# Kernel optimization log

Hardware: AMD Instinct MI355X
Metric: run time of the kernel (lower is better)

Reference implementation:

```python
import jax, jax.numpy as jnp
import numpy as np
import math

B, S, L, D, H, NL, FF, MAXP = 4, 200, 256, 256, 8, 2, 1024, 512
VOC, EDIM, BERT_D, LBL = 50000, 50, 768, 20
DH = D // H
NEG = -1e15


def _pe_table():
    # get_embedding(max_seq_len, hidden, rel_pos_init=0): sinusoidal over 0..2*MAXP
    half = D // 2
    freq = jnp.exp(jnp.arange(half, dtype=jnp.float32) * (-math.log(10000.0) / (half - 1)))
    pos = jnp.arange(2 * MAXP + 1, dtype=jnp.float32)[:, None] * freq[None, :]
    return jnp.concatenate([jnp.sin(pos), jnp.cos(pos)], axis=1)  # [2*MAXP+1, D]


def _ln(x, g, b, eps=1e-5):
    m = x.mean(-1, keepdims=True)
    v = jnp.mean((x - m) ** 2, -1, keepdims=True)
    return (x - m) * jax.lax.rsqrt(v + eps) * g + b


def _forward(lattice, bigrams, seq_len, lex_num, pos_s, pos_e,
             bert_embed, lat_table, big_table, Wc, bc, Wl, bl, W_fus, b_fus,
             Wq, bq, Wk, bk, Wv, bv, Wr, br, u, vb, Wo, bo,
             ln1_g, ln1_b, W1, b1, W2, b2, ln2_g, ln2_b, Wout, bout):
    raw = lat_table[lattice]                                        # [B,L,EDIM]
    big = jnp.pad(big_table[bigrams], ((0, 0), (0, L - S), (0, 0)))  # pad to lattice len
    bert = jnp.pad(bert_embed, ((0, 0), (0, L - S), (0, 0)))
    raw_char = jnp.concatenate([raw, big, bert], -1)                # [B,L,868]
    idx = jnp.arange(L)
    char_mask = idx[None, :] < seq_len[:, None]
    tot_mask = idx[None, :] < (seq_len + lex_num)[:, None]
    lex_mask = tot_mask & (~char_mask)
    # embed_char masked to char positions, embed_lex masked to lexicon positions
    x = (raw_char @ Wc + bc) * char_mask[..., None] + (raw @ Wl + bl) * lex_mask[..., None]

    # four-way relative position fusion ('ff'): relu(Linear(cat[pe_ss,pe_se,pe_es,pe_ee]))
    # computed as sum of four gathered pre-projected tables (same math, no 4D concat)
    pe = _pe_table()
    T = jnp.einsum('pe,keo->kpo', pe, W_fus.reshape(4, D, D))       # [4, 2*MAXP+1, D]
    ss = pos_s[:, :, None] - pos_s[:, None, :] + MAXP
    se = pos_s[:, :, None] - pos_e[:, None, :] + MAXP
    es = pos_e[:, :, None] - pos_s[:, None, :] + MAXP
    ee = pos_e[:, :, None] - pos_e[:, None, :] + MAXP
    rel = jax.nn.relu(T[0][ss] + T[1][se] + T[2][es] + T[3][ee] + b_fus)  # [B,L,L,D]

    scale = 1.0 / math.sqrt(DH)
    for l in range(NL):
        qh = (x @ Wq[l] + bq[l]).reshape(B, L, H, DH).transpose(0, 2, 1, 3)
        kh = (x @ Wk[l] + bk[l]).reshape(B, L, H, DH).transpose(0, 2, 1, 3)
        vh = (x @ Wv[l] + bv[l]).reshape(B, L, H, DH).transpose(0, 2, 1, 3)
        rh = (rel @ Wr[l] + br[l]).reshape(B, L, L, H, DH)
        # Transformer-XL style: A+C with content bias u, B+D with position bias v
        AC = jnp.einsum('bhqd,bhkd->bhqk', qh + u[l][None, :, None, :], kh)
        BD = jnp.einsum('bhqd,bqkhd->bhqk', qh + vb[l][None, :, None, :], rh)
        score = (AC + BD) * scale
        score = jnp.where(tot_mask[:, None, None, :], score, NEG)
        attn = jax.nn.softmax(score, -1)
        out = jnp.einsum('bhqk,bhkd->bhqd', attn, vh).transpose(0, 2, 1, 3).reshape(B, L, D)
        x = _ln(out @ Wo[l] + bo[l] + x, ln1_g[l], ln1_b[l])
        h = jax.nn.relu(x @ W1[l] + b1[l]) @ W2[l] + b2[l]
        x = _ln(h + x, ln2_g[l], ln2_b[l])
    return x[:, :S] @ Wout + bout                                   # emission logits [B,S,LBL]


def setup_inputs() -> dict:
    key = jax.random.key(0)
    ks = jax.random.split(key, 32)
    p = lambda i, sh, s=0.02: jax.random.normal(ks[i], sh, jnp.float32) * s
    inp = {}
    inp['lattice'] = jax.random.randint(ks[0], (B, L), 1, VOC)
    inp['bigrams'] = jax.random.randint(ks[1], (B, S), 1, VOC)
    inp['seq_len'] = jax.random.randint(ks[2], (B,), 150, S + 1)
    inp['lex_num'] = jax.random.randint(ks[3], (B,), 20, L - S + 1)
    s_lex = jax.random.randint(ks[4], (B, L - S), 0, 180)
    e_lex = s_lex + jax.random.randint(ks[5], (B, L - S), 1, 20)
    ar = jnp.broadcast_to(jnp.arange(S), (B, S))
    inp['pos_s'] = jnp.concatenate([ar, s_lex], 1)
    inp['pos_e'] = jnp.concatenate([ar, e_lex], 1)
    inp['target'] = jax.random.randint(ks[6], (B, S), 0, LBL)
    inp['bert_embed'] = p(7, (B, S, BERT_D), 1.0)
    inp['lat_table'] = p(8, (VOC, EDIM), 1.0)
    inp['big_table'] = p(9, (VOC, EDIM), 1.0)
    cin = 2 * EDIM + BERT_D
    inp['Wc'] = p(10, (cin, D)); inp['bc'] = jnp.zeros((D,))
    inp['Wl'] = p(11, (EDIM, D)); inp['bl'] = jnp.zeros((D,))
    inp['W_fus'] = p(12, (4 * D, D)); inp['b_fus'] = jnp.zeros((D,))
    inp['Wq'] = p(13, (NL, D, D)); inp['bq'] = jnp.zeros((NL, D))
    inp['Wk'] = p(14, (NL, D, D)); inp['bk'] = jnp.zeros((NL, D))
    inp['Wv'] = p(15, (NL, D, D)); inp['bv'] = jnp.zeros((NL, D))
    inp['Wr'] = p(16, (NL, D, D)); inp['br'] = jnp.zeros((NL, D))
    inp['u'] = p(17, (NL, H, DH)); inp['vb'] = p(18, (NL, H, DH))
    inp['Wo'] = p(19, (NL, D, D)); inp['bo'] = jnp.zeros((NL, D))
    inp['ln1_g'] = jnp.ones((NL, D)); inp['ln1_b'] = jnp.zeros((NL, D))
    inp['W1'] = p(20, (NL, D, FF)); inp['b1'] = jnp.zeros((NL, FF))
    inp['W2'] = p(21, (NL, FF, D)); inp['b2'] = jnp.zeros((NL, D))
    inp['ln2_g'] = jnp.ones((NL, D)); inp['ln2_b'] = jnp.zeros((NL, D))
    inp['Wout'] = p(22, (D, LBL)); inp['bout'] = jnp.zeros((LBL,))
    return inp


def reference(lattice, bigrams, seq_len, lex_num, pos_s, pos_e, target,
              bert_embed, lat_table, big_table, Wc, bc, Wl, bl, W_fus, b_fus,
              Wq, bq, Wk, bk, Wv, bv, Wr, br, u, vb, Wo, bo,
              ln1_g, ln1_b, W1, b1, W2, b2, ln2_g, ln2_b, Wout, bout):
    # target is consumed by the downstream CRF loss (omitted); emission logits returned
    return _forward(lattice, bigrams, seq_len, lex_num, pos_s, pos_e,
                    bert_embed, lat_table, big_table, Wc, bc, Wl, bl, W_fus, b_fus,
                    Wq, bq, Wk, bk, Wv, bv, Wr, br, u, vb, Wo, bo,
                    ln1_g, ln1_b, W1, b1, W2, b2, ln2_g, ln2_b, Wout, bout)
```

## Files before the change

kernel.cpp:

```cpp
#include <hip/hip_runtime.h>
#include <math.h>

#define NB 4
#define SS 200
#define LT 256
#define DD 256
#define NH 8
#define NLAYER 2
#define FFD 1024
#define BERTD 768
#define NEGINF -1e15f

typedef __attribute__((ext_vector_type(8))) short bf16x8;
typedef __attribute__((ext_vector_type(4))) float f32x4;
typedef __attribute__((ext_vector_type(8))) unsigned short u16x8;

__device__ inline float bf2f(unsigned short h) {
    union { unsigned int u; float f; } v; v.u = ((unsigned int)h) << 16; return v.f;
}
__device__ inline unsigned short f2bf(float x) {
    union { float f; unsigned int u; } v; v.f = x;
    unsigned int r = v.u + 0x7fffu + ((v.u >> 16) & 1u);
    return (unsigned short)(r >> 16);
}
__device__ inline void split2(float x, unsigned short& h, unsigned short& l) {
    h = f2bf(x); l = f2bf(x - bf2f(h));
}

__global__ void gather_v3(const int* __restrict__ lattice, const int* __restrict__ bigrams,
                          const int* __restrict__ seq_len, const int* __restrict__ lex_num,
                          const float* __restrict__ bert, const float* __restrict__ lat_t,
                          const float* __restrict__ big_t,
                          unsigned short* __restrict__ Gh, unsigned short* __restrict__ Gl)
{
    const int row = blockIdx.x, t = threadIdx.x;
    const int b = row >> 8, l = row & 255;
    const int sl = seq_len[b], tl = sl + lex_num[b];
    const float mC = (l < sl) ? 1.f : 0.f;
    const float mL = (l >= sl && l < tl) ? 1.f : 0.f;
    const int lat = lattice[row];
    const int big = (l < SS) ? bigrams[b*SS + l] : 0;
    for (int i = t; i < 1024; i += 256) {
        float v;
        if (i < 50)        v = lat_t[lat*50 + i] * mC;
        else if (i < 100)  v = (l < SS) ? big_t[big*50 + (i-50)] * mC : 0.f;
        else if (i < 868)  v = (l < SS) ? bert[(b*SS + l)*BERTD + (i-100)] * mC : 0.f;
        else if (i < 918)  v = lat_t[lat*50 + (i-868)] * mL;
        else if (i == 918) v = mC;
        else if (i == 919) v = mL;
        else               v = 0.f;
        unsigned short hh, ll; split2(v, hh, ll);
        Gh[(size_t)row*1024 + i] = hh; Gl[(size_t)row*1024 + i] = ll;
    }
}

__global__ void wcomb_kernel(const float* __restrict__ Wc, const float* __restrict__ bc,
                             const float* __restrict__ Wl, const float* __restrict__ bl,
                             float* __restrict__ Wcomb)
{
    const int r = blockIdx.x, t = threadIdx.x;
    float v;
    if (r < 868)       v = Wc[r*DD + t];
    else if (r < 918)  v = Wl[(r-868)*DD + t];
    else if (r == 918) v = bc[t];
    else if (r == 919) v = bl[t];
    else               v = 0.f;
    Wcomb[r*DD + t] = v;
}

__global__ void pe_v3(unsigned short* __restrict__ PEh, unsigned short* __restrict__ PEl)
{
    const int p = blockIdx.x, t = threadIdx.x;
    float v = 0.f;
    if (p <= 1024) {
        const float fr = expf(-(float)(t & 127) * (9.210340371976184f / 127.0f));
        const float arg = (float)p * fr;
        v = (t < 128) ? sinf(arg) : cosf(arg);
    }
    unsigned short hh, ll; split2(v, hh, ll);
    PEh[p*DD + t] = hh; PEl[p*DD + t] = ll;
}

__global__ void smallpack(const float* __restrict__ bq, const float* __restrict__ bk,
                          const float* __restrict__ bv, const float* __restrict__ b_fus,
                          float* __restrict__ bqkv, float* __restrict__ bfus4)
{
    const int t = threadIdx.x;
    for (int l = 0; l < NLAYER; ++l) {
        bqkv[l*768 + t]       = bq[l*DD + t];
        bqkv[l*768 + 256 + t] = bk[l*DD + t];
        bqkv[l*768 + 512 + t] = bv[l*DD + t];
    }
    bfus4[t] = b_fus[t];
    bfus4[256 + t] = 0.f; bfus4[512 + t] = 0.f; bfus4[768 + t] = 0.f;
}

__global__ void vrbias_kernel(const float* __restrict__ vb, const float* __restrict__ Wr,
                              float* __restrict__ bias_vr)
{
    const int lh = blockIdx.x, t = threadIdx.x;
    const int l = lh >> 3, h = lh & 7;
    float acc = 0.f;
    #pragma unroll 8
    for (int d = 0; d < 32; ++d)
        acc += vb[l*DD + h*32 + d] * Wr[(size_t)l*DD*DD + (h*32 + d)*DD + t];
    bias_vr[lh*DD + t] = acc;
}

__global__ void trans_all(const float* __restrict__ Wcomb, const float* __restrict__ Wq,
                          const float* __restrict__ Wk, const float* __restrict__ Wv,
                          const float* __restrict__ Wo, const float* __restrict__ W1,
                          const float* __restrict__ W2, const float* __restrict__ Wfus,
                          const float* __restrict__ Wr,
                          unsigned short* WcombT_h, unsigned short* WcombT_l,
                          unsigned short* WqkvT_h,  unsigned short* WqkvT_l,
                          unsigned short* WoT_h,    unsigned short* WoT_l,
                          unsigned short* W1T_h,    unsigned short* W1T_l,
                          unsigned short* W2T_h,    unsigned short* W2T_l,
                          unsigned short* WfusT_h,  unsigned short* WfusT_l,
                          unsigned short* WrB_h,    unsigned short* WrB_l)
{
    const int z = blockIdx.z, y = blockIdx.y, tx = blockIdx.x, t = threadIdx.x;
    const float* src; unsigned short *dh, *dl; int K, N;
    switch (z) {
        case 0: if (y) return; K = 1024; N = 256; src = Wcomb; dh = WcombT_h; dl = WcombT_l; break;
        case 1: { if (y >= 6) return; int l = y/3, s = y%3; K = 256; N = 256;
                  src = (s==0 ? Wq : s==1 ? Wk : Wv) + l*65536;
                  dh = WqkvT_h + (l*768 + s*256)*256; dl = WqkvT_l + (l*768 + s*256)*256; } break;
        case 2: if (y >= 2) return; K = 256; N = 256;  src = Wo + y*65536;  dh = WoT_h + y*65536;  dl = WoT_l + y*65536;  break;
        case 3: if (y >= 2) return; K = 256; N = 1024; src = W1 + y*262144; dh = W1T_h + y*262144; dl = W1T_l + y*262144; break;
        case 4: if (y >= 2) return; K = 1024; N = 256; src = W2 + y*262144; dh = W2T_h + y*262144; dl = W2T_l + y*262144; break;
        case 5: if (y >= 4) return; K = 256; N = 256;  src = Wfus + y*65536; dh = WfusT_h + y*65536; dl = WfusT_l + y*65536; break;
        case 6: { if (y >= 16) return; int l = y >> 3, h = y & 7; K = 32; N = 256;
                  src = Wr + (size_t)l*65536 + h*32*256;
                  dh = WrB_h + y*8192; dl = WrB_l + y*8192; } break;
        default: return;
    }
    const int tiles_x = N >> 5;
    const int tn = tx % tiles_x, tk = tx / tiles_x;
    if (tk >= (K >> 5)) return;
    __shared__ float s[32][33];
    const int lr = t >> 5, lc = t & 31;
    #pragma unroll
    for (int i = 0; i < 4; ++i)
        s[lr + 8*i][lc] = src[(size_t)(tk*32 + lr + 8*i)*N + tn*32 + lc];
    __syncthreads();
    #pragma unroll
    for (int i = 0; i < 4; ++i) {
        const int n = tn*32 + lr + 8*i, k = tk*32 + lc;
        unsigned short hh, ll; split2(s[lc][lr + 8*i], hh, ll);
        dh[(size_t)n*K + k] = hh;
        dl[(size_t)n*K + k] = ll;
    }
}

template<int BK, bool RELU, bool EMIT>
__global__ __launch_bounds__(256) void gemm_v3(
    const unsigned short* __restrict__ Ah, const unsigned short* __restrict__ Al,
    const unsigned short* __restrict__ Bh, const unsigned short* __restrict__ Bl,
    const float* __restrict__ bias, const float* __restrict__ resid,
    float* __restrict__ C, unsigned short* __restrict__ Ch, unsigned short* __restrict__ Cl,
    int M, int N, int K, int lda, int ldc, int aZ, int bZ, int cZ, int biasZ)
{
    constexpr int LDK = BK + 8;
    __shared__ unsigned short AhS[64*LDK], AlS[64*LDK];
    __shared__ unsigned short BhS[64*LDK], BlS[64*LDK];
    const int z = blockIdx.z;
    Ah += (size_t)z * aZ; Al += (size_t)z * aZ;
    Bh += (size_t)z * bZ; Bl += (size_t)z * bZ;
    C  += (size_t)z * cZ;
    if (EMIT) { Ch += (size_t)z * cZ; Cl += (size_t)z * cZ; }
    if (bias) bias += (size_t)z * biasZ;

    const int t = threadIdx.x;
    const int row0 = blockIdx.y * 64, col0 = blockIdx.x * 64;
    const int lane = t & 63, w = t >> 6;
    const int wm = w >> 1, wn = w & 1;
    const int fr = lane & 15, fq = lane >> 4;
    const int sr = t >> 2, sc0 = (t & 3) * (BK/4);

    f32x4 acc[2][2];
    #pragma unroll
    for (int i = 0; i < 2; ++i)
        #pragma unroll
        for (int j = 0; j < 2; ++j) acc[i][j] = (f32x4){0.f, 0.f, 0.f, 0.f};

    for (int k0 = 0; k0 < K; k0 += BK) {
        #pragma unroll
        for (int i = 0; i < BK/32; ++i) {
            const int c = sc0 + i*8;
            *(u16x8*)&AhS[sr*LDK + c] = *(const u16x8*)&Ah[(size_t)(row0+sr)*lda + k0 + c];
            *(u16x8*)&AlS[sr*LDK + c] = *(const u16x8*)&Al[(size_t)(row0+sr)*lda + k0 + c];
            *(u16x8*)&BhS[sr*LDK + c] = *(const u16x8*)&Bh[(size_t)(col0+sr)*K + k0 + c];
            *(u16x8*)&BlS[sr*LDK + c] = *(const u16x8*)&Bl[(size_t)(col0+sr)*K + k0 + c];
        }
        __syncthreads();
        #pragma unroll
        for (int ks = 0; ks < BK/32; ++ks) {
            const int ko = ks*32 + fq*8;
            const bf16x8 ah0 = *(const bf16x8*)&AhS[(wm*32 + fr)*LDK + ko];
            const bf16x8 ah1 = *(const bf16x8*)&AhS[(wm*32 + 16 + fr)*LDK + ko];
            const bf16x8 al0 = *(const bf16x8*)&AlS[(wm*32 + fr)*LDK + ko];
            const bf16x8 al1 = *(const bf16x8*)&AlS[(wm*32 + 16 + fr)*LDK + ko];
            #pragma unroll
            for (int nt = 0; nt < 2; ++nt) {
                const int nb = (wn*32 + nt*16 + fr)*LDK + ko;
                const bf16x8 bh = *(const bf16x8*)&BhS[nb];
                const bf16x8 bl = *(const bf16x8*)&BlS[nb];
                acc[0][nt] = __builtin_amdgcn_mfma_f32_16x16x32_bf16(ah0, bh, acc[0][nt], 0, 0, 0);
                acc[0][nt] = __builtin_amdgcn_mfma_f32_16x16x32_bf16(ah0, bl, acc[0][nt], 0, 0, 0);
                acc[0][nt] = __builtin_amdgcn_mfma_f32_16x16x32_bf16(al0, bh, acc[0][nt], 0, 0, 0);
                acc[1][nt] = __builtin_amdgcn_mfma_f32_16x16x32_bf16(ah1, bh, acc[1][nt], 0, 0, 0);
                acc[1][nt] = __builtin_amdgcn_mfma_f32_16x16x32_bf16(ah1, bl, acc[1][nt], 0, 0, 0);
                acc[1][nt] = __builtin_amdgcn_mfma_f32_16x16x32_bf16(al1, bh, acc[1][nt], 0, 0, 0);
            }
        }
        __syncthreads();
    }
    #pragma unroll
    for (int mt = 0; mt < 2; ++mt) {
        #pragma unroll
        for (int nt = 0; nt < 2; ++nt) {
            const int gcol = col0 + wn*32 + nt*16 + fr;
            const float bv = bias ? bias[gcol] : 0.f;
            #pragma unroll
            for (int r = 0; r < 4; ++r) {
                const int grow = row0 + wm*32 + mt*16 + fq*4 + r;
                float v = acc[mt][nt][r] + bv;
                if (resid) v += resid[(size_t)grow*ldc + gcol];
                if (RELU)  v = fmaxf(v, 0.f);
                C[(size_t)grow*ldc + gcol] = v;
                if (EMIT) {
                    unsigned short hh, ll; split2(v, hh, ll);
                    Ch[(size_t)grow*ldc + gcol] = hh;
                    Cl[(size_t)grow*ldc + gcol] = ll;
                }
            }
        }
    }
}

__global__ void rcc_kernel(const float* __restrict__ Tn, float* __restrict__ Rcc)
{
    const int p = blockIdx.x, t = threadIdx.x;
    const float v = Tn[(size_t)p*1024 + t] + Tn[(size_t)p*1024 + 256 + t]
                  + Tn[(size_t)p*1024 + 512 + t] + Tn[(size_t)p*1024 + 768 + t];
    Rcc[p*DD + t] = fmaxf(v, 0.f);
}

__global__ __launch_bounds__(256) void attn_v3(
    const float* __restrict__ qkvb, const float* __restrict__ qr,
    const float* __restrict__ Tn, const float* __restrict__ Rcc,
    const int* __restrict__ pos_s, const int* __restrict__ pos_e,
    const int* __restrict__ seq_len, const int* __restrict__ lex_num,
    const float* __restrict__ u, float* __restrict__ ob,
    unsigned short* __restrict__ obh, unsigned short* __restrict__ obl)
{
    __shared__ float qrl[NH][260];
    __shared__ float qu[256];
    __shared__ float sc[NH][264];
    __shared__ float red[1024];
    const int t = threadIdx.x;
    const int row = blockIdx.x;
    const int b = row >> 8, q = row & 255;
    const int totlen = seq_len[b] + lex_num[b];
    if (q >= SS && q >= totlen) {
        ob[row*DD + t] = 0.f; obh[row*DD + t] = 0; obl[row*DD + t] = 0;
        return;
    }
    qu[t] = qkvb[(size_t)row*768 + t] + u[t];
    #pragma unroll
    for (int h = 0; h < NH; ++h) qrl[h][t] = qr[(size_t)row*2048 + h*256 + t];
    const int ps_q = pos_s[row], pe_q = pos_e[row];
    const int* psb = pos_s + b*LT;
    const int* peb = pos_e + b*LT;
    __syncthreads();

    const int w = t >> 6, lane = t & 63;
    const int kl = lane >> 1, half = lane & 1, e0 = half*128;
    #pragma unroll
    for (int it = 0; it < 2; ++it) {
        const int K0 = (w + it*4) * 32;
        const int kg = K0 + kl;
        if (kg < totlen) {
            float a[8] = {0.f,0.f,0.f,0.f,0.f,0.f,0.f,0.f};
            const int sk = psb[kg], ek = peb[kg];
            if (q < SS && kg < SS) {
                const float4* rp = (const float4*)(Rcc + (ps_q - sk + 512)*DD + e0);
                for (int e4 = 0; e4 < 32; ++e4) {
                    const float4 r4 = rp[e4];
                    #pragma unroll
                    for (int h = 0; h < 8; ++h) {
                        const float4 q4 = *(const float4*)&qrl[h][e0 + e4*4];
                        a[h] += r4.x*q4.x + r4.y*q4.y + r4.z*q4.z + r4.w*q4.w;
                    }
                }
            } else {
                const float4* t0p = (const float4*)(Tn + (size_t)(ps_q - sk + 512)*1024 + e0);
                const float4* t1p = (const float4*)(Tn + (size_t)(ps_q - ek + 512)*1024 + 256 + e0);
                const float4* t2p = (const float4*)(Tn + (size_t)(pe_q - sk + 512)*1024 + 512 + e0);
                const float4* t3p = (const float4*)(Tn + (size_t)(pe_q - ek + 512)*1024 + 768 + e0);
                for (int e4 = 0; e4 < 32; ++e4) {
                    const float4 va = t0p[e4], vb2 = t1p[e4], vc = t2p[e4], vd = t3p[e4];
                    float4 r4;
                    r4.x = fmaxf(va.x + vb2.x + vc.x + vd.x, 0.f);
                    r4.y = fmaxf(va.y + vb2.y + vc.y + vd.y, 0.f);
                    r4.z = fmaxf(va.z + vb2.z + vc.z + vd.z, 0.f);
                    r4.w = fmaxf(va.w + vb2.w + vc.w + vd.w, 0.f);
                    #pragma unroll
                    for (int h = 0; h < 8; ++h) {
                        const float4 q4 = *(const float4*)&qrl[h][e0 + e4*4];
                        a[h] += r4.x*q4.x + r4.y*q4.y + r4.z*q4.z + r4.w*q4.w;
                    }
                }
            }
            {
                const float* kp = qkvb + (size_t)(b*LT + kg)*768 + 256;
                #pragma unroll
                for (int hh = 0; hh < 4; ++hh) {
                    const int h = half*4 + hh;
                    float ac = 0.f;
                    #pragma unroll
                    for (int d4 = 0; d4 < 8; ++d4) {
                        const float4 kv = *(const float4*)&kp[h*32 + d4*4];
                        const float4 qv = *(const float4*)&qu[h*32 + d4*4];
                        ac += kv.x*qv.x + kv.y*qv.y + kv.z*qv.z + kv.w*qv.w;
                    }
                    a[h] += ac;
                }
            }
            #pragma unroll
            for (int h = 0; h < 8; ++h) a[h] += __shfl_xor(a[h], 1);
            if (half == 0) {
                #pragma unroll
                for (int h = 0; h < 8; ++h) sc[h][kg] = a[h] * 0.17677669529663687f;
            }
        } else if (half == 0) {
            #pragma unroll
            for (int h = 0; h < 8; ++h) sc[h][kg] = NEGINF;
        }
    }
    __syncthreads();
    {
        const int g = t >> 5, ln = t & 31;
        float vals[8];
        float m = -INFINITY;
        #pragma unroll
        for (int i = 0; i < 8; ++i) {
            const int kidx = ln + 32*i;
            vals[i] = (kidx < totlen) ? sc[g][kidx] : NEGINF;
            m = fmaxf(m, vals[i]);
        }
        #pragma unroll
        for (int off = 16; off >= 1; off >>= 1) m = fmaxf(m, __shfl_xor(m, off, 32));
        float sum = 0.f;
        #pragma unroll
        for (int i = 0; i < 8; ++i) { vals[i] = expf(vals[i] - m); sum += vals[i]; }
        #pragma unroll
        for (int off = 16; off >= 1; off >>= 1) sum += __shfl_xor(sum, off, 32);
        const float inv = 1.0f / sum;
        #pragma unroll
        for (int i = 0; i < 8; ++i) sc[g][ln + 32*i] = vals[i] * inv;
    }
    __syncthreads();
    {
        const int j4 = (t & 63)*4, kr = t >> 6;
        const int h = j4 >> 5;
        float4 acc = make_float4(0.f, 0.f, 0.f, 0.f);
        const float* vp = qkvb + (size_t)(b*LT)*768 + 512 + j4;
        for (int k = kr; k < totlen; k += 4) {
            const float p = sc[h][k];
            const float4 v = *(const float4*)&vp[(size_t)k*768];
            acc.x += p*v.x; acc.y += p*v.y; acc.z += p*v.z; acc.w += p*v.w;
        }
        *(float4*)&red[kr*256 + j4] = acc;
    }
    __syncthreads();
    {
        const float v = red[t] + red[256 + t] + red[512 + t] + red[768 + t];
        ob[row*DD + t] = v;
        unsigned short hh, ll; split2(v, hh, ll);
        obh[row*DD + t] = hh; obl[row*DD + t] = ll;
    }
}

template<bool EMIT>
__global__ void ln_v3(const float* __restrict__ in, const float* __restrict__ g,
                      const float* __restrict__ bb, float* __restrict__ out,
                      unsigned short* __restrict__ oh, unsigned short* __restrict__ ol)
{
    __shared__ float red[4];
    const int t = threadIdx.x, row = blockIdx.x;
    const float v = in[row*DD + t];
    float s = v;
    #pragma unroll
    for (int off = 32; off >= 1; off >>= 1) s += __shfl_xor(s, off, 64);
    if ((t & 63) == 0) red[t >> 6] = s;
    __syncthreads();
    const float m = (red[0] + red[1] + red[2] + red[3]) * (1.0f/256.0f);
    __syncthreads();
    const float d = v - m;
    float s2 = d*d;
    #pragma unroll
    for (int off = 32; off >= 1; off >>= 1) s2 += __shfl_xor(s2, off, 64);
    if ((t & 63) == 0) red[t >> 6] = s2;
    __syncthreads();
    const float var = (red[0] + red[1] + red[2] + red[3]) * (1.0f/256.0f);
    const float o = d * rsqrtf(var + 1e-5f) * g[t] + bb[t];
    out[row*DD + t] = o;
    if (EMIT) {
        unsigned short hh, ll; split2(o, hh, ll);
        oh[row*DD + t] = hh; ol[row*DD + t] = ll;
    }
}

__global__ void out_kernel(const float* __restrict__ x, const float* __restrict__ Wout,
                           const float* __restrict__ bout, float* __restrict__ out)
{
    __shared__ float xs[256];
    const int t = threadIdx.x, row = blockIdx.x;
    const int b = row / SS, s = row % SS;
    const float* xr = x + (b*LT + s)*DD;
    for (int i = t; i < DD; i += 64) xs[i] = xr[i];
    __syncthreads();
    if (t < 20) {
        float acc = bout[t];
        for (int d = 0; d < DD; ++d) acc += xs[d] * Wout[d*20 + t];
        out[row*20 + t] = acc;
    }
}

extern "C" void kernel_launch(void* const* d_in, const int* in_sizes, int n_in,
                              void* d_out, int out_size, void* d_ws, size_t ws_size,
                              hipStream_t stream)
{
    const int*   lattice = (const int*)d_in[0];
    const int*   bigrams = (const int*)d_in[1];
    const int*   seq_len = (const int*)d_in[2];
    const int*   lex_num = (const int*)d_in[3];
    const int*   pos_s   = (const int*)d_in[4];
    const int*   pos_e   = (const int*)d_in[5];
    const float* bert    = (const float*)d_in[7];
    const float* lat_t   = (const float*)d_in[8];
    const float* big_t   = (const float*)d_in[9];
    const float* Wc      = (const float*)d_in[10];
    const float* bc      = (const float*)d_in[11];
    const float* Wl      = (const float*)d_in[12];
    const float* bl      = (const float*)d_in[13];
    const float* W_fus   = (const float*)d_in[14];
    const float* b_fus   = (const float*)d_in[15];
    const float* Wq      = (const float*)d_in[16];
    const float* bq      = (const float*)d_in[17];
    const float* Wk      = (const float*)d_in[18];
    const float* bk      = (const float*)d_in[19];
    const float* Wv      = (const float*)d_in[20];
    const float* bv      = (const float*)d_in[21];
    const float* Wr      = (const float*)d_in[22];
    const float* u_bias  = (const float*)d_in[24];
    const float* v_bias  = (const float*)d_in[25];
    const float* Wo      = (const float*)d_in[26];
    const float* bo      = (const float*)d_in[27];
    const float* ln1g    = (const float*)d_in[28];
    const float* ln1b    = (const float*)d_in[29];
    const float* W1      = (const float*)d_in[30];
    const float* b1      = (const float*)d_in[31];
    const float* W2      = (const float*)d_in[32];
    const float* b2      = (const float*)d_in[33];
    const float* ln2g    = (const float*)d_in[34];
    const float* ln2b    = (const float*)d_in[35];
    const float* Wout    = (const float*)d_in[36];
    const float* bout    = (const float*)d_in[37];

    float* ws = (float*)d_ws;
    float* qkvb = ws;  ws += NB*LT*768;
    float* ob   = ws;  ws += NB*LT*DD;
    float* t1   = ws;  ws += NB*LT*DD;
    float* x2   = ws;  ws += NB*LT*DD;
    float* t2   = ws;  ws += NB*LT*DD;
    float* hb   = ws;  ws += NB*LT*FFD;
    float* x    = ws;  ws += NB*LT*DD;
    float* Tn   = ws;  ws += 1088*1024;
    float* Rcc  = ws;  ws += 1025*DD;
    float* qr   = ws;  ws += NB*LT*NH*DD;
    float* Wcomb= ws;  ws += 1024*DD;
    float* bqkv = ws;  ws += NLAYER*768;
    float* bfus4= ws;  ws += 1024;
    float* bias_vr = ws; ws += NLAYER*NH*DD;
    unsigned short* us = (unsigned short*)ws;
    unsigned short* xh  = us; us += 1024*256;
    unsigned short* xl  = us; us += 1024*256;
    unsigned short* x2h = us; us += 1024*256;
    unsigned short* x2l = us; us += 1024*256;
    unsigned short* qkvbh = us; us += 1024*768;
    unsigned short* qkvbl = us; us += 1024*768;
    unsigned short* hbh = us; us += 1024*1024;
    unsigned short* hbl = us; us += 1024*1024;
    unsigned short* obh = us; us += 1024*256;
    unsigned short* obl = us; us += 1024*256;
    unsigned short* WcombT_h = us; us += 256*1024;
    unsigned short* WcombT_l = us; us += 256*1024;
    unsigned short* WqkvT_h  = us; us += NLAYER*768*256;
    unsigned short* WqkvT_l  = us; us += NLAYER*768*256;
    unsigned short* WoT_h    = us; us += NLAYER*256*256;
    unsigned short* WoT_l    = us; us += NLAYER*256*256;
    unsigned short* W1T_h    = us; us += NLAYER*1024*256;
    unsigned short* W1T_l    = us; us += NLAYER*1024*256;
    unsigned short* W2T_h    = us; us += NLAYER*256*1024;
    unsigned short* W2T_l    = us; us += NLAYER*256*1024;
    unsigned short* WfusT_h  = us; us += 1024*256;
    unsigned short* WfusT_l  = us; us += 1024*256;
    unsigned short* WrB_h    = us; us += NLAYER*NH*256*32;
    unsigned short* WrB_l    = us; us += NLAYER*NH*256*32;
    unsigned short* Gh  = hbh;
    unsigned short* Gl  = hbl;
    unsigned short* PEh = (unsigned short*)t1;
    unsigned short* PEl = (unsigned short*)t2;

    const int M = NB*LT;

    gather_v3<<<M, 256, 0, stream>>>(lattice, bigrams, seq_len, lex_num,
                                     bert, lat_t, big_t, Gh, Gl);
    wcomb_kernel<<<1024, 256, 0, stream>>>(Wc, bc, Wl, bl, Wcomb);
    pe_v3<<<1088, 256, 0, stream>>>(PEh, PEl);
    smallpack<<<1, 256, 0, stream>>>(bq, bk, bv, b_fus, bqkv, bfus4);
    vrbias_kernel<<<NLAYER*NH, 256, 0, stream>>>(v_bias, Wr, bias_vr);
    trans_all<<<dim3(256, 16, 7), 256, 0, stream>>>(Wcomb, Wq, Wk, Wv, Wo, W1, W2, W_fus, Wr,
        WcombT_h, WcombT_l, WqkvT_h, WqkvT_l, WoT_h, WoT_l,
        W1T_h, W1T_l, W2T_h, W2T_l, WfusT_h, WfusT_l, WrB_h, WrB_l);

    gemm_v3<64,false,false><<<dim3(16, 17), 256, 0, stream>>>(
        PEh, PEl, WfusT_h, WfusT_l, bfus4, nullptr, Tn, nullptr, nullptr,
        1088, 1024, 256, 256, 1024, 0, 0, 0, 0);
    rcc_kernel<<<1025, 256, 0, stream>>>(Tn, Rcc);

    gemm_v3<64,false,true><<<dim3(4, 16), 256, 0, stream>>>(
        Gh, Gl, WcombT_h, WcombT_l, nullptr, nullptr, x, xh, xl,
        M, 256, 1024, 1024, 256, 0, 0, 0, 0);

    for (int l = 0; l < NLAYER; ++l) {
        gemm_v3<64,false,true><<<dim3(12, 16), 256, 0, stream>>>(
            xh, xl, WqkvT_h + l*768*256, WqkvT_l + l*768*256, bqkv + l*768, nullptr,
            qkvb, qkvbh, qkvbl, M, 768, 256, 256, 768, 0, 0, 0, 0);
        gemm_v3<32,false,false><<<dim3(4, 16, 8), 256, 0, stream>>>(
            qkvbh, qkvbl, WrB_h + l*8*8192, WrB_l + l*8*8192, bias_vr + l*8*256, nullptr,
            qr, nullptr, nullptr, M, 256, 32, 768, 2048, 32, 8192, 256, 256);
        attn_v3<<<M, 256, 0, stream>>>(qkvb, qr, Tn, Rcc, pos_s, pos_e,
                                       seq_len, lex_num, u_bias + l*DD, ob, obh, obl);
        gemm_v3<64,false,false><<<dim3(4, 16), 256, 0, stream>>>(
            obh, obl, WoT_h + l*65536, WoT_l + l*65536, bo + l*DD, x,
            t1, nullptr, nullptr, M, 256, 256, 256, 256, 0, 0, 0, 0);
        ln_v3<true><<<M, 256, 0, stream>>>(t1, ln1g + l*DD, ln1b + l*DD, x2, x2h, x2l);
        gemm_v3<64,true,true><<<dim3(16, 16), 256, 0, stream>>>(
            x2h, x2l, W1T_h + l*262144, W1T_l + l*262144, b1 + l*FFD, nullptr,
            hb, hbh, hbl, M, FFD, 256, 256, 1024, 0, 0, 0, 0);
        gemm_v3<64,false,false><<<dim3(4, 16), 256, 0, stream>>>(
            hbh, hbl, W2T_h + l*262144, W2T_l + l*262144, b2 + l*DD, x2,
            t2, nullptr, nullptr, M, 256, 1024, 1024, 256, 0, 0, 0, 0);
        ln_v3<true><<<M, 256, 0, stream>>>(t2, ln2g + l*DD, ln2b + l*DD, x, xh, xl);
    }
    out_kernel<<<NB*SS, 64, 0, stream>>>(x, Wout, bout, (float*)d_out);
}
```

Baseline: 566.6 us.

## Precompute char-char relative scores with a GEMM over the position-difference table

For char-char query/key pairs, the relative-position score now comes from a batched split-bf16 GEMM. It multiplies each query's qr rows by a window of the ReLU'd combined table, Dcc, indexed by position difference. The attention kernel then just looks the value up instead of doing a per-key 256-wide dot product against gathered rows. The remaining lexicon pairs use a restructured tiled loop: it stages 32 relative rows in shared memory, spreads the dot products across threads and reduces through shared memory. This replaces a lot of redundant gather-and-dot work with tensor-core matrix work, at the cost of an extra kernel, a large Dcc buffer and more shared memory per block. The lookup assumes pos_s equals the index for char tokens.

```diff
diff --git a/kernel.cpp b/kernel.cpp
--- a/kernel.cpp
+++ b/kernel.cpp
@@ -10,6 +10,7 @@
 #define FFD 1024
 #define BERTD 768
 #define NEGINF -1e15f
+#define SCL 0.17677669529663687f
 
 typedef __attribute__((ext_vector_type(8))) short bf16x8;
 typedef __attribute__((ext_vector_type(4))) float f32x4;
@@ -240,107 +241,142 @@
     }
 }
 
-__global__ void rcc_kernel(const float* __restrict__ Tn, float* __restrict__ Rcc)
+__global__ void rcc_split(const float* __restrict__ Tn,
+                          unsigned short* __restrict__ Rh, unsigned short* __restrict__ Rl)
 {
     const int p = blockIdx.x, t = threadIdx.x;
     const float v = Tn[(size_t)p*1024 + t] + Tn[(size_t)p*1024 + 256 + t]
                   + Tn[(size_t)p*1024 + 512 + t] + Tn[(size_t)p*1024 + 768 + t];
-    Rcc[p*DD + t] = fmaxf(v, 0.f);
-}
-
-__global__ __launch_bounds__(256) void attn_v3(
+    unsigned short hh, ll; split2(fmaxf(v, 0.f), hh, ll);
+    Rh[p*DD + t] = hh; Rl[p*DD + t] = ll;
+}
+
+__global__ __launch_bounds__(256) void attn_v4(
     const float* __restrict__ qkvb, const float* __restrict__ qr,
-    const float* __restrict__ Tn, const float* __restrict__ Rcc,
+    const float* __restrict__ Tn, const float* __restrict__ Dcc,
     const int* __restrict__ pos_s, const int* __restrict__ pos_e,
     const int* __restrict__ seq_len, const int* __restrict__ lex_num,
     const float* __restrict__ u, float* __restrict__ ob,
     unsigned short* __restrict__ obh, unsigned short* __restrict__ obl)
 {
+    __shared__ float qu[256];
     __shared__ float qrl[NH][260];
-    __shared__ float qu[256];
     __shared__ float sc[NH][264];
-    __shared__ float red[1024];
-    const int t = threadIdx.x;
-    const int row = blockIdx.x;
+    __shared__ float acb[NH][264];
+    __shared__ float relb[32][260];
+    __shared__ float red[2048];
+    float* DccL = &relb[0][0];
+
+    const int t = threadIdx.x, row = blockIdx.x;
     const int b = row >> 8, q = row & 255;
     const int totlen = seq_len[b] + lex_num[b];
     if (q >= SS && q >= totlen) {
         ob[row*DD + t] = 0.f; obh[row*DD + t] = 0; obl[row*DD + t] = 0;
         return;
     }
+    const bool qc = (q < SS);
+    const int gstart = qc ? SS : 0;
+
     qu[t] = qkvb[(size_t)row*768 + t] + u[t];
-    #pragma unroll
-    for (int h = 0; h < NH; ++h) qrl[h][t] = qr[(size_t)row*2048 + h*256 + t];
+    if (totlen > gstart) {
+        #pragma unroll
+        for (int h = 0; h < NH; ++h) qrl[h][t] = qr[(size_t)row*2048 + h*256 + t];
+    }
+    if (qc && t < SS) {
+        #pragma unroll
+        for (int h = 0; h < NH; ++h)
+            DccL[h*SS + t] = Dcc[((size_t)h*1024 + row)*448 + q + t];
+    }
     const int ps_q = pos_s[row], pe_q = pos_e[row];
     const int* psb = pos_s + b*LT;
     const int* peb = pos_e + b*LT;
     __syncthreads();
 
-    const int w = t >> 6, lane = t & 63;
-    const int kl = lane >> 1, half = lane & 1, e0 = half*128;
-    #pragma unroll
-    for (int it = 0; it < 2; ++it) {
-        const int K0 = (w + it*4) * 32;
-        const int kg = K0 + kl;
-        if (kg < totlen) {
-            float a[8] = {0.f,0.f,0.f,0.f,0.f,0.f,0.f,0.f};
-            const int sk = psb[kg], ek = peb[kg];
-            if (q < SS && kg < SS) {
-                const float4* rp = (const float4*)(Rcc + (ps_q - sk + 512)*DD + e0);
-                for (int e4 = 0; e4 < 32; ++e4) {
-                    const float4 r4 = rp[e4];
+    {
+        const int h = t & 7, k0 = t >> 3;
+        const float4* qp = (const float4*)&qu[h*32];
+        #pragma unroll
+        for (int pass = 0; pass < 8; ++pass) {
+            const int kg = pass*32 + k0;
+            if (kg < totlen) {
+                const float4* kp = (const float4*)&qkvb[(size_t)(b*LT + kg)*768 + 256 + h*32];
+                float ac = 0.f;
+                #pragma unroll
+                for (int d4 = 0; d4 < 8; ++d4) {
+                    const float4 kv = kp[d4], qv = qp[d4];
+                    ac += kv.x*qv.x + kv.y*qv.y + kv.z*qv.z + kv.w*qv.w;
+                }
+                if (qc && kg < SS) sc[h][kg] = (ac + DccL[h*SS + (SS-1) - kg]) * SCL;
+                else               acb[h][kg] = ac;
+            } else {
+                sc[h][kg] = NEGINF;
+            }
+        }
+    }
+    __syncthreads();
+
+    const int gs0 = gstart & ~31;
+    for (int K0 = gs0; K0 < totlen; K0 += 32) {
+        {
+            const int r = t >> 3, c4 = (t & 7)*4;
+            const int kg = K0 + r;
+            if (kg >= gstart && kg < totlen) {
+                const int sk = psb[kg], ek = peb[kg];
+                const float* t0 = Tn + (size_t)(ps_q - sk + 512)*1024;
+                const float* t1 = Tn + (size_t)(ps_q - ek + 512)*1024 + 256;
+                const float* t2 = Tn + (size_t)(pe_q - sk + 512)*1024 + 512;
+                const float* t3 = Tn + (size_t)(pe_q - ek + 512)*1024 + 768;
+                #pragma unroll
+                for (int i = 0; i < 8; ++i) {
+                    const int e = i*32 + c4;
+                    const float4 a = *(const float4*)&t0[e];
+                    const float4 bb = *(const float4*)&t1[e];
+                    const float4 c = *(const float4*)&t2[e];
+                    const float4 d = *(const float4*)&t3[e];
+                    float4 v;
+                    v.x = fmaxf(a.x + bb.x + c.x + d.x, 0.f);
+                    v.y = fmaxf(a.y + bb.y + c.y + d.y, 0.f);
+                    v.z = fmaxf(a.z + bb.z + c.z + d.z, 0.f);
+                    v.w = fmaxf(a.w + bb.w + c.w + d.w, 0.f);
+                    *(float4*)&relb[r][e] = v;
+                }
+            }
+        }
+        __syncthreads();
+        {
+            const int dk = t & 31, seg = t >> 5;
+            const int kg = K0 + dk;
+            if (kg >= gstart && kg < totlen) {
+                float a[8] = {0.f,0.f,0.f,0.f,0.f,0.f,0.f,0.f};
+                const int e0 = seg*32;
+                #pragma unroll
+                for (int e4 = 0; e4 < 8; ++e4) {
+                    const float4 r4 = *(const float4*)&relb[dk][e0 + e4*4];
                     #pragma unroll
                     for (int h = 0; h < 8; ++h) {
                         const float4 q4 = *(const float4*)&qrl[h][e0 + e4*4];
                         a[h] += r4.x*q4.x + r4.y*q4.y + r4.z*q4.z + r4.w*q4.w;
                     }
                 }
-            } else {
-                const float4* t0p = (const float4*)(Tn + (size_t)(ps_q - sk + 512)*1024 + e0);
-                const float4* t1p = (const float4*)(Tn + (size_t)(ps_q - ek + 512)*1024 + 256 + e0);
-                const float4* t2p = (const float4*)(Tn + (size_t)(pe_q - sk + 512)*1024 + 512 + e0);
-                const float4* t3p = (const float4*)(Tn + (size_t)(pe_q - ek + 512)*1024 + 768 + e0);
-                for (int e4 = 0; e4 < 32; ++e4) {
-                    const float4 va = t0p[e4], vb2 = t1p[e4], vc = t2p[e4], vd = t3p[e4];
-                    float4 r4;
-                    r4.x = fmaxf(va.x + vb2.x + vc.x + vd.x, 0.f);
-                    r4.y = fmaxf(va.y + vb2.y + vc.y + vd.y, 0.f);
-                    r4.z = fmaxf(va.z + vb2.z + vc.z + vd.z, 0.f);
-                    r4.w = fmaxf(va.w + vb2.w + vc.w + vd.w, 0.f);
-                    #pragma unroll
-                    for (int h = 0; h < 8; ++h) {
-                        const float4 q4 = *(const float4*)&qrl[h][e0 + e4*4];
-                        a[h] += r4.x*q4.x + r4.y*q4.y + r4.z*q4.z + r4.w*q4.w;
-                    }
-                }
+                float4* rb = (float4*)&red[(seg*32 + dk)*8];
+                rb[0] = make_float4(a[0], a[1], a[2], a[3]);
+                rb[1] = make_float4(a[4], a[5], a[6], a[7]);
             }
-            {
-                const float* kp = qkvb + (size_t)(b*LT + kg)*768 + 256;
+        }
+        __syncthreads();
+        {
+            const int k = t >> 3, h = t & 7;
+            const int kg = K0 + k;
+            if (kg >= gstart && kg < totlen) {
+                float s = 0.f;
                 #pragma unroll
-                for (int hh = 0; hh < 4; ++hh) {
-                    const int h = half*4 + hh;
-                    float ac = 0.f;
-                    #pragma unroll
-                    for (int d4 = 0; d4 < 8; ++d4) {
-                        const float4 kv = *(const float4*)&kp[h*32 + d4*4];
-                        const float4 qv = *(const float4*)&qu[h*32 + d4*4];
-                        ac += kv.x*qv.x + kv.y*qv.y + kv.z*qv.z + kv.w*qv.w;
-                    }
-                    a[h] += ac;
-                }
+                for (int g = 0; g < 8; ++g) s += red[g*256 + t];
+                sc[h][kg] = (s + acb[h][kg]) * SCL;
             }
-            #pragma unroll
-            for (int h = 0; h < 8; ++h) a[h] += __shfl_xor(a[h], 1);
-            if (half == 0) {
-                #pragma unroll
-                for (int h = 0; h < 8; ++h) sc[h][kg] = a[h] * 0.17677669529663687f;
-            }
-        } else if (half == 0) {
-            #pragma unroll
-            for (int h = 0; h < 8; ++h) sc[h][kg] = NEGINF;
-        }
-    }
-    __syncthreads();
+        }
+        __syncthreads();
+    }
+
     {
         const int g = t >> 5, ln = t & 31;
         float vals[8];
@@ -480,8 +516,8 @@
     float* hb   = ws;  ws += NB*LT*FFD;
     float* x    = ws;  ws += NB*LT*DD;
     float* Tn   = ws;  ws += 1088*1024;
-    float* Rcc  = ws;  ws += 1025*DD;
     float* qr   = ws;  ws += NB*LT*NH*DD;
+    float* Dcc  = ws;  ws += 8*1024*448;
     float* Wcomb= ws;  ws += 1024*DD;
     float* bqkv = ws;  ws += NLAYER*768;
     float* bfus4= ws;  ws += 1024;
@@ -497,6 +533,10 @@
     unsigned short* hbl = us; us += 1024*1024;
     unsigned short* obh = us; us += 1024*256;
     unsigned short* obl = us; us += 1024*256;
+    unsigned short* qrh = us; us += 1024*2048;
+    unsigned short* qrl = us; us += 1024*2048;
+    unsigned short* Rcch = us; us += 1025*256;
+    unsigned short* Rccl = us; us += 1025*256;
     unsigned short* WcombT_h = us; us += 256*1024;
     unsigned short* WcombT_l = us; us += 256*1024;
     unsigned short* WqkvT_h  = us; us += NLAYER*768*256;
@@ -531,7 +571,7 @@
     gemm_v3<64,false,false><<<dim3(16, 17), 256, 0, stream>>>(
         PEh, PEl, WfusT_h, WfusT_l, bfus4, nullptr, Tn, nullptr, nullptr,
         1088, 1024, 256, 256, 1024, 0, 0, 0, 0);
-    rcc_kernel<<<1025, 256, 0, stream>>>(Tn, Rcc);
+    rcc_split<<<1025, 256, 0, stream>>>(Tn, Rcch, Rccl);
 
     gemm_v3<64,false,true><<<dim3(4, 16), 256, 0, stream>>>(
         Gh, Gl, WcombT_h, WcombT_l, nullptr, nullptr, x, xh, xl,
@@ -541,10 +581,13 @@
         gemm_v3<64,false,true><<<dim3(12, 16), 256, 0, stream>>>(
             xh, xl, WqkvT_h + l*768*256, WqkvT_l + l*768*256, bqkv + l*768, nullptr,
             qkvb, qkvbh, qkvbl, M, 768, 256, 256, 768, 0, 0, 0, 0);
-        gemm_v3<32,false,false><<<dim3(4, 16, 8), 256, 0, stream>>>(
+        gemm_v3<32,false,true><<<dim3(4, 16, 8), 256, 0, stream>>>(
             qkvbh, qkvbl, WrB_h + l*8*8192, WrB_l + l*8*8192, bias_vr + l*8*256, nullptr,
-            qr, nullptr, nullptr, M, 256, 32, 768, 2048, 32, 8192, 256, 256);
-        attn_v3<<<M, 256, 0, stream>>>(qkvb, qr, Tn, Rcc, pos_s, pos_e,
+            qr, qrh, qrl, M, 256, 32, 768, 2048, 32, 8192, 256, 256);
+        gemm_v3<64,false,false><<<dim3(7, 16, 8), 256, 0, stream>>>(
+            qrh, qrl, Rcch + 313*256, Rccl + 313*256, nullptr, nullptr,
+            Dcc, nullptr, nullptr, M, 448, 256, 2048, 448, 256, 0, 1024*448, 0);
+        attn_v4<<<M, 256, 0, stream>>>(qkvb, qr, Tn, Dcc, pos_s, pos_e,
                                        seq_len, lex_num, u_bias + l*DD, ob, obh, obl);
         gemm_v3<64,false,false><<<dim3(4, 16), 256, 0, stream>>>(
             obh, obl, WoT_h + l*65536, WoT_l + l*65536, bo + l*DD, x,
```

Measured after the change: 492.6 us. 13.1% less time.
